# Optimization experiments

Hardware: AMD Instinct MI355X
Metric: run time of the kernel (lower is better)

Reference implementation:

```python
import jax, jax.numpy as jnp
import numpy as np

EOS_ID = 2
PAD_ID = 0


def setup_inputs() -> dict:
    key = jax.random.key(0)
    ks = jax.random.split(key, 10)
    B, E, H, V, T = 64, 512, 512, 32000, 20
    features = jax.random.normal(ks[0], (B, E), dtype=jnp.float32)
    captions = jax.random.randint(ks[1], (B, T), 0, V)            # unused in policy branch
    lengths = jax.random.randint(ks[2], (B,), 1, T + 1)
    lengths = lengths.at[0].set(T)                                 # make max(lengths) == 20 deterministic
    # parameters (match torch init scales roughly)
    embed_W = jax.random.uniform(ks[3], (V, E), jnp.float32, -0.1, 0.1)
    s = 1.0 / np.sqrt(H)
    W_ih = jax.random.uniform(ks[4], (4 * H, E), jnp.float32, -s, s)
    W_hh = jax.random.uniform(ks[5], (4 * H, H), jnp.float32, -s, s)
    b_ih = jax.random.uniform(ks[6], (4 * H,), jnp.float32, -s, s)
    b_hh = jax.random.uniform(ks[7], (4 * H,), jnp.float32, -s, s)
    linear_W = jax.random.uniform(ks[8], (V, H), jnp.float32, -0.1, 0.1)
    linear_b = jnp.zeros((V,), jnp.float32)
    return {"features": features, "captions": captions, "lengths": lengths,
            "use_policy": 1, "embed_W": embed_W, "W_ih": W_ih, "W_hh": W_hh,
            "b_ih": b_ih, "b_hh": b_hh, "linear_W": linear_W, "linear_b": linear_b}


def _lstm_cell(x, h, c, W_ih, W_hh, b_ih, b_hh):
    # PyTorch gate order: i, f, g, o
    gates = x @ W_ih.T + b_ih + h @ W_hh.T + b_hh        # [B, 4H]
    i, f, g, o = jnp.split(gates, 4, axis=-1)
    i, f, o = jax.nn.sigmoid(i), jax.nn.sigmoid(f), jax.nn.sigmoid(o)
    g = jnp.tanh(g)
    c = f * c + i * g
    h = o * jnp.tanh(c)
    return h, c


def reference(features, captions, lengths, use_policy, embed_W, W_ih, W_hh,
              b_ih, b_hh, linear_W, linear_b):
    # LSTM decode with categorical sampling, stopping per-example at EOS (id 2)
    # and padding remaining steps with id 0 / log_prob 0. The original loops
    # over batch and time with batch-size-1 kernels; here we batch + lax.scan.
    B, H = features.shape[0], W_hh.shape[1]
    T = int(jnp.max(lengths))                            # concrete at trace setup
    step_keys = jax.random.split(jax.random.key(42), T)

    def step(carry, key_t):
        h, c, x, done = carry
        h, c = _lstm_cell(x, h, c, W_ih, W_hh, b_ih, b_hh)
        logits = h @ linear_W.T + linear_b               # [B, V]
        logp = jax.nn.log_softmax(logits, axis=-1)
        tok = jax.random.categorical(key_t, logits)      # [B] int32
        lp = jnp.take_along_axis(logp, tok[:, None], axis=1)[:, 0]
        ids_rec = jnp.where(done, PAD_ID, tok)
        lp_rec = jnp.where(done, 0.0, lp)
        done = done | ((tok == EOS_ID) & ~done)          # EOS token itself is recorded
        x = embed_W[tok]                                 # next-step input embedding
        return (h, c, x, done), (ids_rec, lp_rec)

    init = (jnp.zeros((B, H), features.dtype), jnp.zeros((B, H), features.dtype),
            features, jnp.zeros((B,), bool))
    _, (ids, logps) = jax.lax.scan(step, init, step_keys)
    sampled_ids = jnp.transpose(ids)                     # [B, T]
    saved_log_probs = jnp.transpose(logps)               # [B, T]
    return sampled_ids, saved_log_probs
```

## Files before the change

### kernel.cpp

```cpp
#include <hip/hip_runtime.h>
#include <hip/hip_bf16.h>
#include <stdint.h>
#include <float.h>

#define BB 64
#define EE 512
#define HH 512
#define VV 32000
#define TT 20
#define INV2048 0.00048828125f

typedef _Float16 f16x8 __attribute__((ext_vector_type(8)));
typedef float f32x4 __attribute__((ext_vector_type(4)));

__device__ __host__ __forceinline__ void tf2x32(uint32_t k0, uint32_t k1, uint32_t x0, uint32_t x1,
                                                uint32_t& o0, uint32_t& o1) {
  const uint32_t k2 = k0 ^ k1 ^ 0x1BD11BDAu;
  x0 += k0; x1 += k1;
#define RND(R) { x0 += x1; x1 = (x1 << R) | (x1 >> (32 - R)); x1 ^= x0; }
  RND(13) RND(15) RND(26) RND(6)
  x0 += k1; x1 += k2 + 1u;
  RND(17) RND(29) RND(16) RND(24)
  x0 += k2; x1 += k0 + 2u;
  RND(13) RND(15) RND(26) RND(6)
  x0 += k0; x1 += k1 + 3u;
  RND(17) RND(29) RND(16) RND(24)
  x0 += k1; x1 += k2 + 4u;
  RND(13) RND(15) RND(26) RND(6)
  x0 += k2; x1 += k0 + 5u;
#undef RND
  o0 = x0; o1 = x1;
}

__device__ __forceinline__ float gumbel_for(uint32_t k1t, uint32_t k2t, uint32_t idx) {
  uint32_t o0, o1; tf2x32(k1t, k2t, 0u, idx, o0, o1);
  uint32_t bits = o0 ^ o1;
  uint32_t mant = bits >> 9;
  float f = __uint_as_float(0x3f800000u | mant) - 1.0f;
  float u = mant ? f : 1.1754943508222875e-38f;
  return -logf(-logf(u));
}

struct Part { float bv; int bix; float blog; float m; float s; };

__device__ __forceinline__ void part_combine(Part& P, const Part& Q) {
  if (Q.bv > P.bv || (Q.bv == P.bv && Q.bix < P.bix)) { P.bv = Q.bv; P.bix = Q.bix; P.blog = Q.blog; }
  if (Q.m > P.m) { P.s = P.s * expf(P.m - Q.m) + Q.s; P.m = Q.m; }
  else           { P.s += Q.s * expf(Q.m - P.m); }
}

__global__ __launch_bounds__(256) void k_init(float* __restrict__ hA, float* __restrict__ cT,
                                              int* __restrict__ done) {
  int i = blockIdx.x * 256 + threadIdx.x;
  if (i < HH * BB) { hA[i] = 0.f; cT[i] = 0.f; }
  if (i < BB) done[i] = 0;
}

__global__ __launch_bounds__(256) void k_gates(const float* __restrict__ xin,
                                               const float* __restrict__ hT,
                                               const float* __restrict__ Wih,
                                               const float* __restrict__ Whh,
                                               float* __restrict__ gatesP) {
  const int jt = blockIdx.x;
  const int kc = blockIdx.y;
  const int tx = threadIdx.x;
  __shared__ float a[64][64];
  __shared__ float wj[64][68];
  const int bi = (tx & 15) * 4;
  const int ji = (tx >> 4) * 4;
  float acc[4][4] = {};
  const float* Wsrc = (kc < 4) ? Wih : Whh;
  for (int s = 0; s < 2; ++s) {
    const int kg = kc * 128 + s * 64;
    if (kc < 4) {
      #pragma unroll
      for (int r = 0; r < 4; ++r) {
        int fi = r * 256 + tx;
        int b = fi >> 4, k4 = (fi & 15) * 4;
        const float4 v = *(const float4*)(xin + b * EE + kg + k4);
        a[k4 + 0][b] = v.x; a[k4 + 1][b] = v.y; a[k4 + 2][b] = v.z; a[k4 + 3][b] = v.w;
      }
    } else {
      #pragma unroll
      for (int r = 0; r < 4; ++r) {
        int fi = r * 256 + tx;
        int row = fi >> 4, c4 = (fi & 15) * 4;
        *(float4*)(&a[row][c4]) = *(const float4*)(hT + (kg - 512 + row) * BB + c4);
      }
    }
    const int kcol = kg & 511;
    #pragma unroll
    for (int r = 0; r < 4; ++r) {
      int fi = r * 256 + tx;
      int j = fi >> 4, k4 = (fi & 15) * 4;
      const float4 v = *(const float4*)(Wsrc + (size_t)(jt * 64 + j) * EE + kcol + k4);
      wj[k4 + 0][j] = v.x; wj[k4 + 1][j] = v.y; wj[k4 + 2][j] = v.z; wj[k4 + 3][j] = v.w;
    }
    __syncthreads();
    #pragma unroll 8
    for (int kk = 0; kk < 64; ++kk) {
      const float4 av = *(const float4*)(&a[kk][bi]);
      const float4 wv = *(const float4*)(&wj[kk][ji]);
      const float avx[4] = {av.x, av.y, av.z, av.w};
      const float wvx[4] = {wv.x, wv.y, wv.z, wv.w};
      #pragma unroll
      for (int jj = 0; jj < 4; ++jj)
        #pragma unroll
        for (int bb = 0; bb < 4; ++bb)
          acc[jj][bb] = fmaf(wvx[jj], avx[bb], acc[jj][bb]);
    }
    __syncthreads();
  }
  #pragma unroll
  for (int jj = 0; jj < 4; ++jj) {
    float4 o = make_float4(acc[jj][0], acc[jj][1], acc[jj][2], acc[jj][3]);
    *(float4*)(gatesP + ((size_t)kc * 2048 + jt * 64 + ji + jj) * BB + bi) = o;
  }
}

__global__ __launch_bounds__(256) void k_lstm_update(const float* __restrict__ gatesP,
                                                     const float* __restrict__ b_ih,
                                                     const float* __restrict__ b_hh,
                                                     float* __restrict__ cT,
                                                     float* __restrict__ hT) {
  const int blk = blockIdx.x;
  const int tx = threadIdx.x;
  const int b = tx & 63;
  const int dk = tx >> 6;
  #pragma unroll
  for (int r = 0; r < 2; ++r) {
    const int k = blk * 8 + dk + r * 4;
    float g[4];
    #pragma unroll
    for (int gi = 0; gi < 4; ++gi) {
      const int j = gi * 512 + k;
      float s = 0.f;
      #pragma unroll
      for (int kc = 0; kc < 8; ++kc) s += gatesP[((size_t)kc * 2048 + j) * BB + b];
      g[gi] = s + b_ih[j] + b_hh[j];
    }
    const float ig = 1.f / (1.f + expf(-g[0]));
    const float fg = 1.f / (1.f + expf(-g[1]));
    const float gg = tanhf(g[2]);
    const float og = 1.f / (1.f + expf(-g[3]));
    const float c = fg * cT[k * BB + b] + ig * gg;
    cT[k * BB + b] = c;
    hT[k * BB + b] = og * tanhf(c);
  }
}

__global__ __launch_bounds__(256) void k_lstm_update_frag(const float* __restrict__ gatesP,
                                                          const float* __restrict__ b_ih,
                                                          const float* __restrict__ b_hh,
                                                          float* __restrict__ cT,
                                                          float* __restrict__ hT,
                                                          _Float16* __restrict__ hfh,
                                                          _Float16* __restrict__ hfl) {
  const int blk = blockIdx.x;
  const int tx = threadIdx.x;
  const int b = tx & 63;
  const int dk = tx >> 6;
  #pragma unroll
  for (int r = 0; r < 2; ++r) {
    const int k = blk * 8 + dk + r * 4;
    float g[4];
    #pragma unroll
    for (int gi = 0; gi < 4; ++gi) {
      const int j = gi * 512 + k;
      float s = 0.f;
      #pragma unroll
      for (int kc = 0; kc < 8; ++kc) s += gatesP[((size_t)kc * 2048 + j) * BB + b];
      g[gi] = s + b_ih[j] + b_hh[j];
    }
    const float ig = 1.f / (1.f + expf(-g[0]));
    const float fg = 1.f / (1.f + expf(-g[1]));
    const float gg = tanhf(g[2]);
    const float og = 1.f / (1.f + expf(-g[3]));
    const float c = fg * cT[k * BB + b] + ig * gg;
    cT[k * BB + b] = c;
    const float h = og * tanhf(c);
    hT[k * BB + b] = h;
    const _Float16 hh = (_Float16)h;
    const _Float16 hl = (_Float16)((h - (float)hh) * 2048.0f);
    const int cc = k >> 5, kr = k & 31;
    const int lane = (kr >> 3) * 16 + (b & 15), j = kr & 7, nb = b >> 4;
    const int idx = ((cc * 4 + nb) * 64 + lane) * 8 + j;
    hfh[idx] = hh; hfl[idx] = hl;
  }
}

__global__ __launch_bounds__(256) void k_convW(const float* __restrict__ LW,
                                               _Float16* __restrict__ Wh,
                                               _Float16* __restrict__ Wl) {
  const int t = blockIdx.x * 256 + threadIdx.x;
  const int v = t >> 6, kq = t & 63;
  const float4 f0 = *(const float4*)(LW + (size_t)v * HH + kq * 8);
  const float4 f1 = *(const float4*)(LW + (size_t)v * HH + kq * 8 + 4);
  const int vb = v >> 4, m = v & 15;
  const int c = kq >> 2, lh = kq & 3;
  const size_t o = (((size_t)vb * 16 + c) * 64 + lh * 16 + m) * 8;
  const float f[8] = {f0.x, f0.y, f0.z, f0.w, f1.x, f1.y, f1.z, f1.w};
  f16x8 hi, lo;
  #pragma unroll
  for (int j = 0; j < 8; ++j) {
    const _Float16 h = (_Float16)f[j];
    hi[j] = h;
    lo[j] = (_Float16)((f[j] - (float)h) * 2048.0f);
  }
  *(f16x8*)(Wh + o) = hi;
  *(f16x8*)(Wl + o) = lo;
}

__global__ __launch_bounds__(64) void k_logits3(const f16x8* __restrict__ Wh,
                                                const f16x8* __restrict__ Wl,
                                                const f16x8* __restrict__ hfh,
                                                const f16x8* __restrict__ hfl,
                                                const float* __restrict__ lb,
                                                uint32_t k1t, uint32_t k2t,
                                                float4* __restrict__ pf4,
                                                int* __restrict__ pidx) {
  const int vt = blockIdx.x;
  const int lane = threadIdx.x;
  const f32x4 zero = {0.f, 0.f, 0.f, 0.f};
  f32x4 aH[4] = {zero, zero, zero, zero};
  f32x4 aM[4] = {zero, zero, zero, zero};
  #pragma unroll 4
  for (int c = 0; c < 16; ++c) {
    const f16x8 wh = Wh[((size_t)vt * 16 + c) * 64 + lane];
    const f16x8 wl = Wl[((size_t)vt * 16 + c) * 64 + lane];
    #pragma unroll
    for (int nb = 0; nb < 4; ++nb) {
      const f16x8 bh = hfh[(c * 4 + nb) * 64 + lane];
      const f16x8 bl = hfl[(c * 4 + nb) * 64 + lane];
      aH[nb] = __builtin_amdgcn_mfma_f32_16x16x32_f16(wh, bh, aH[nb], 0, 0, 0);
      aM[nb] = __builtin_amdgcn_mfma_f32_16x16x32_f16(wh, bl, aM[nb], 0, 0, 0);
      aM[nb] = __builtin_amdgcn_mfma_f32_16x16x32_f16(wl, bh, aM[nb], 0, 0, 0);
    }
  }
  const int v0 = vt * 16 + ((lane >> 4) << 2);
  const float4 bias = *(const float4*)(lb + v0);
  const float bb4[4] = {bias.x, bias.y, bias.z, bias.w};
  Part P[4];
  #pragma unroll
  for (int nb = 0; nb < 4; ++nb) {
    const int b = nb * 16 + (lane & 15);
    float lg = aH[nb][0] + aM[nb][0] * INV2048 + bb4[0];
    Part p;
    p.bv = lg + gumbel_for(k1t, k2t, (uint32_t)(b * VV + v0));
    p.bix = v0; p.blog = lg; p.m = lg; p.s = 1.0f;
    #pragma unroll
    for (int reg = 1; reg < 4; ++reg) {
      float lg2 = aH[nb][reg] + aM[nb][reg] * INV2048 + bb4[reg];
      float pe = lg2 + gumbel_for(k1t, k2t, (uint32_t)(b * VV + v0 + reg));
      if (pe > p.bv) { p.bv = pe; p.bix = v0 + reg; p.blog = lg2; }
      if (lg2 > p.m) { p.s = p.s * expf(p.m - lg2) + 1.f; p.m = lg2; }
      else           { p.s += expf(lg2 - p.m); }
    }
    P[nb] = p;
  }
  #pragma unroll
  for (int msk = 16; msk <= 32; msk <<= 1) {
    #pragma unroll
    for (int nb = 0; nb < 4; ++nb) {
      Part Q;
      Q.bv   = __shfl_xor(P[nb].bv, msk, 64);
      Q.bix  = __shfl_xor(P[nb].bix, msk, 64);
      Q.blog = __shfl_xor(P[nb].blog, msk, 64);
      Q.m    = __shfl_xor(P[nb].m, msk, 64);
      Q.s    = __shfl_xor(P[nb].s, msk, 64);
      part_combine(P[nb], Q);
    }
  }
  if (lane < 16) {
    #pragma unroll
    for (int nb = 0; nb < 4; ++nb) {
      const int b = nb * 16 + lane;
      pf4[(size_t)vt * BB + b] = make_float4(P[nb].bv, P[nb].blog, P[nb].m, P[nb].s);
      pidx[vt * BB + b] = P[nb].bix;
    }
  }
}

__global__ __launch_bounds__(128) void k_logits2(const float* __restrict__ hT,
                                                 const float* __restrict__ LW,
                                                 const float* __restrict__ lb,
                                                 uint32_t k1t, uint32_t k2t,
                                                 float4* __restrict__ pf4,
                                                 int* __restrict__ pidx) {
  const int vt = blockIdx.x;
  const int tx = threadIdx.x;
  __shared__ float lds[5120];
  float* wTs = lds;
  const int vthr = tx & 15;
  const int bthr = tx >> 4;
  const int vi = vthr * 2;
  const int bi = bthr * 8;
  const int vq = tx >> 4;
  const int ks = tx & 15;
  float acc[2][8] = {};
  for (int kt = 0; kt < 8; ++kt) {
    const int kg = kt * 64;
    #pragma unroll
    for (int s = 0; s < 4; ++s) {
      const int kk = ks + 16 * s;
      const size_t rb = (size_t)(vt * 32 + 4 * vq) * HH + kg + kk;
      float w0 = LW[rb];
      float w1 = LW[rb + HH];
      float w2 = LW[rb + 2 * HH];
      float w3 = LW[rb + 3 * HH];
      const int ph = (4 * vq) ^ (4 * (kk & 7));
      *(float4*)&wTs[kk * 32 + ph] = make_float4(w0, w1, w2, w3);
    }
    __syncthreads();
    #pragma unroll 4
    for (int kk = 0; kk < 64; ++kk) {
      const float* hrow = hT + (size_t)(kg + kk) * BB;
      const float4 h0 = *(const float4*)(hrow + bi);
      const float4 h1 = *(const float4*)(hrow + bi + 4);
      const float2 wv = *(const float2*)&wTs[kk * 32 + (vi ^ (4 * (kk & 7)))];
      acc[0][0] = fmaf(wv.x, h0.x, acc[0][0]); acc[0][1] = fmaf(wv.x, h0.y, acc[0][1]);
      acc[0][2] = fmaf(wv.x, h0.z, acc[0][2]); acc[0][3] = fmaf(wv.x, h0.w, acc[0][3]);
      acc[0][4] = fmaf(wv.x, h1.x, acc[0][4]); acc[0][5] = fmaf(wv.x, h1.y, acc[0][5]);
      acc[0][6] = fmaf(wv.x, h1.z, acc[0][6]); acc[0][7] = fmaf(wv.x, h1.w, acc[0][7]);
      acc[1][0] = fmaf(wv.y, h0.x, acc[1][0]); acc[1][1] = fmaf(wv.y, h0.y, acc[1][1]);
      acc[1][2] = fmaf(wv.y, h0.z, acc[1][2]); acc[1][3] = fmaf(wv.y, h0.w, acc[1][3]);
      acc[1][4] = fmaf(wv.y, h1.x, acc[1][4]); acc[1][5] = fmaf(wv.y, h1.y, acc[1][5]);
      acc[1][6] = fmaf(wv.y, h1.z, acc[1][6]); acc[1][7] = fmaf(wv.y, h1.w, acc[1][7]);
    }
    __syncthreads();
  }
  const int v0g = vt * 32 + vi;
  const float bias0 = lb[v0g];
  const float bias1 = lb[v0g + 1];
  float* red = lds;
  #pragma unroll
  for (int bb = 0; bb < 8; ++bb) {
    const int b = bi + bb;
    const float lg0 = acc[0][bb] + bias0;
    const float lg1 = acc[1][bb] + bias1;
    Part p;
    p.bv = lg0 + gumbel_for(k1t, k2t, (uint32_t)(b * VV + v0g));
    p.bix = v0g; p.blog = lg0;
    const float pe1 = lg1 + gumbel_for(k1t, k2t, (uint32_t)(b * VV + v0g + 1));
    if (pe1 > p.bv) { p.bv = pe1; p.bix = v0g + 1; p.blog = lg1; }
    if (lg0 >= lg1) { p.m = lg0; p.s = 1.f + expf(lg1 - lg0); }
    else            { p.m = lg1; p.s = 1.f + expf(lg0 - lg1); }
    const int slot = (b * 16 + vthr) * 5;
    red[slot + 0] = p.bv; red[slot + 1] = __int_as_float(p.bix); red[slot + 2] = p.blog;
    red[slot + 3] = p.m;  red[slot + 4] = p.s;
  }
  __syncthreads();
  if (tx < 64) {
    const int b = tx;
    Part P;
    { const int s0 = (b * 16) * 5;
      P.bv = red[s0]; P.bix = __float_as_int(red[s0 + 1]); P.blog = red[s0 + 2];
      P.m = red[s0 + 3]; P.s = red[s0 + 4]; }
    #pragma unroll
    for (int c = 1; c < 16; ++c) {
      const int s0 = (b * 16 + c) * 5;
      Part Q; Q.bv = red[s0]; Q.bix = __float_as_int(red[s0 + 1]); Q.blog = red[s0 + 2];
      Q.m = red[s0 + 3]; Q.s = red[s0 + 4];
      part_combine(P, Q);
    }
    pf4[(size_t)vt * BB + b] = make_float4(P.bv, P.blog, P.m, P.s);
    pidx[vt * BB + b] = P.bix;
  }
}

__global__ __launch_bounds__(256) void k_sample2(const float4* __restrict__ pf4,
                                                 const int* __restrict__ pidx,
                                                 const float* __restrict__ embW,
                                                 int* __restrict__ done,
                                                 float* __restrict__ x,
                                                 float* __restrict__ out,
                                                 int step, int nvt) {
  const int b = blockIdx.x;
  const int tx = threadIdx.x;
  __shared__ float red[256 * 5];
  __shared__ int stok;
  Part p; p.bv = -FLT_MAX; p.bix = 0x7fffffff; p.blog = 0.f; p.m = -FLT_MAX; p.s = 0.f;
  for (int vt = tx; vt < nvt; vt += 256) {
    float4 q = pf4[(size_t)vt * BB + b];
    Part Q; Q.bv = q.x; Q.blog = q.y; Q.m = q.z; Q.s = q.w; Q.bix = pidx[vt * BB + b];
    part_combine(p, Q);
  }
  red[tx * 5 + 0] = p.bv; red[tx * 5 + 1] = __int_as_float(p.bix); red[tx * 5 + 2] = p.blog;
  red[tx * 5 + 3] = p.m;  red[tx * 5 + 4] = p.s;
  __syncthreads();
  for (int st = 128; st > 0; st >>= 1) {
    if (tx < st) {
      const int s0 = tx * 5, s1 = (tx + st) * 5;
      Part P, Q;
      P.bv = red[s0]; P.bix = __float_as_int(red[s0 + 1]); P.blog = red[s0 + 2]; P.m = red[s0 + 3]; P.s = red[s0 + 4];
      Q.bv = red[s1]; Q.bix = __float_as_int(red[s1 + 1]); Q.blog = red[s1 + 2]; Q.m = red[s1 + 3]; Q.s = red[s1 + 4];
      part_combine(P, Q);
      red[s0] = P.bv; red[s0 + 1] = __int_as_float(P.bix); red[s0 + 2] = P.blog; red[s0 + 3] = P.m; red[s0 + 4] = P.s;
    }
    __syncthreads();
  }
  if (tx == 0) {
    const int tok = __float_as_int(red[1]);
    const float blog = red[2], M = red[3], S = red[4];
    const float lp = blog - (M + logf(S));
    const int dn = done[b];
    out[b * TT + step] = dn ? 0.0f : (float)tok;
    out[BB * TT + b * TT + step] = dn ? 0.0f : lp;
    done[b] = dn | (tok == 2);
    stok = tok;
  }
  __syncthreads();
  const int tok = stok;
  for (int e = tx; e < EE; e += 256) x[b * EE + e] = embW[(size_t)tok * EE + e];
}

extern "C" void kernel_launch(void* const* d_in, const int* in_sizes, int n_in,
                              void* d_out, int out_size, void* d_ws, size_t ws_size,
                              hipStream_t stream) {
  const float* features = (const float*)d_in[0];
  const float* embW     = (const float*)d_in[4];
  const float* Wih      = (const float*)d_in[5];
  const float* Whh      = (const float*)d_in[6];
  const float* bih      = (const float*)d_in[7];
  const float* bhh      = (const float*)d_in[8];
  const float* LW       = (const float*)d_in[9];
  const float* lb       = (const float*)d_in[10];
  float* out = (float*)d_out;

  uint32_t keys[TT][2];
  for (int t = 0; t < TT; ++t) tf2x32(0u, 42u, 0u, (uint32_t)t, keys[t][0], keys[t][1]);

  float* ws = (float*)d_ws;
  float* hA = ws;
  float* hB = ws + 32768;
  float* cT = ws + 65536;
  float* x  = ws + 98304;

  if (ws_size >= (size_t)73000000) {
    float*  gatesP = ws + 131072;
    float4* pf4    = (float4*)(ws + 1179648);
    int*    pidx   = (int*)(ws + 1691648);
    int*    done   = (int*)(ws + 1819648);
    _Float16* hfh  = (_Float16*)(ws + 1819712);
    _Float16* hfl  = (_Float16*)(ws + 1836096);
    _Float16* Whi  = (_Float16*)(ws + 1852480);
    _Float16* Wlo  = (_Float16*)(ws + 10044480);

    k_convW<<<dim3(8000), dim3(256), 0, stream>>>(LW, Whi, Wlo);
    k_init<<<dim3(128), dim3(256), 0, stream>>>(hA, cT, done);
    const float* hin = hA;
    float* hout = hB;
    for (int t = 0; t < TT; ++t) {
      const float* xin = (t == 0) ? features : x;
      k_gates<<<dim3(32, 8), dim3(256), 0, stream>>>(xin, hin, Wih, Whh, gatesP);
      k_lstm_update_frag<<<dim3(64), dim3(256), 0, stream>>>(gatesP, bih, bhh, cT, hout, hfh, hfl);
      k_logits3<<<dim3(2000), dim3(64), 0, stream>>>((const f16x8*)Whi, (const f16x8*)Wlo,
                                                     (const f16x8*)hfh, (const f16x8*)hfl,
                                                     lb, keys[t][0], keys[t][1], pf4, pidx);
      k_sample2<<<dim3(64), dim3(256), 0, stream>>>(pf4, pidx, embW, done, x, out, t, 2000);
      const float* tmp = hout; hout = (float*)hin; hin = tmp;
    }
  } else {
    float*  gatesP = ws + 131072;
    float4* pf4    = (float4*)(ws + 131072 + 1048576);
    int*    pidx   = (int*)(ws + 131072 + 1048576 + 256000);
    int*    done   = (int*)(ws + 131072 + 1048576 + 256000 + 64000);

    k_init<<<dim3(128), dim3(256), 0, stream>>>(hA, cT, done);
    const float* hin = hA;
    float* hout = hB;
    for (int t = 0; t < TT; ++t) {
      const float* xin = (t == 0) ? features : x;
      k_gates<<<dim3(32, 8), dim3(256), 0, stream>>>(xin, hin, Wih, Whh, gatesP);
      k_lstm_update<<<dim3(64), dim3(256), 0, stream>>>(gatesP, bih, bhh, cT, hout);
      k_logits2<<<dim3(1000), dim3(128), 0, stream>>>(hout, LW, lb, keys[t][0], keys[t][1], pf4, pidx);
      k_sample2<<<dim3(64), dim3(256), 0, stream>>>(pf4, pidx, embW, done, x, out, t, 1000);
      const float* tmp = hout; hout = (float*)hin; hin = tmp;
    }
  }
}
```

Before: 1.112 ms.

## Use 4-wave logits blocks with in-block reduction and LDS-staged weight conversion

The logits kernel now runs four waves per block, each handling one 16-vocab tile. The waves combine their partial softmax/argmax results through LDS, so only 500 partials per batch row go to the sampling kernel instead of 2000. It also prefetches the next weight chunk in registers and splits the middle-term MFMA accumulators into two chains to shorten dependency stalls. The weight conversion kernel stages tiles through LDS so its global reads and writes coalesce. In exchange the logits kernel adds a __syncthreads, LDS use and more registers per block.

```diff
diff --git a/kernel.cpp b/kernel.cpp
--- a/kernel.cpp
+++ b/kernel.cpp
@@ -189,53 +189,72 @@
   }
 }
 
-__global__ __launch_bounds__(256) void k_convW(const float* __restrict__ LW,
-                                               _Float16* __restrict__ Wh,
-                                               _Float16* __restrict__ Wl) {
-  const int t = blockIdx.x * 256 + threadIdx.x;
-  const int v = t >> 6, kq = t & 63;
-  const float4 f0 = *(const float4*)(LW + (size_t)v * HH + kq * 8);
-  const float4 f1 = *(const float4*)(LW + (size_t)v * HH + kq * 8 + 4);
-  const int vb = v >> 4, m = v & 15;
-  const int c = kq >> 2, lh = kq & 3;
-  const size_t o = (((size_t)vb * 16 + c) * 64 + lh * 16 + m) * 8;
-  const float f[8] = {f0.x, f0.y, f0.z, f0.w, f1.x, f1.y, f1.z, f1.w};
-  f16x8 hi, lo;
-  #pragma unroll
-  for (int j = 0; j < 8; ++j) {
-    const _Float16 h = (_Float16)f[j];
-    hi[j] = h;
-    lo[j] = (_Float16)((f[j] - (float)h) * 2048.0f);
-  }
-  *(f16x8*)(Wh + o) = hi;
-  *(f16x8*)(Wl + o) = lo;
-}
-
-__global__ __launch_bounds__(64) void k_logits3(const f16x8* __restrict__ Wh,
-                                                const f16x8* __restrict__ Wl,
-                                                const f16x8* __restrict__ hfh,
-                                                const f16x8* __restrict__ hfl,
-                                                const float* __restrict__ lb,
-                                                uint32_t k1t, uint32_t k2t,
-                                                float4* __restrict__ pf4,
-                                                int* __restrict__ pidx) {
-  const int vt = blockIdx.x;
-  const int lane = threadIdx.x;
+__global__ __launch_bounds__(256) void k_convW2(const float* __restrict__ LW,
+                                                _Float16* __restrict__ Wh,
+                                                _Float16* __restrict__ Wl) {
+  const int bv = blockIdx.x, bk = blockIdx.y;
+  const int tx = threadIdx.x;
+  __shared__ float lds[64][65];
+  #pragma unroll
+  for (int r = 0; r < 4; ++r) {
+    const int fi = r * 256 + tx;
+    const int vl = fi >> 4, k4 = (fi & 15) * 4;
+    const float4 v = *(const float4*)(LW + (size_t)(bv * 64 + vl) * HH + bk * 64 + k4);
+    lds[vl][k4] = v.x; lds[vl][k4 + 1] = v.y; lds[vl][k4 + 2] = v.z; lds[vl][k4 + 3] = v.w;
+  }
+  __syncthreads();
+  #pragma unroll
+  for (int r = 0; r < 2; ++r) {
+    const int u = r * 256 + tx;
+    const int frag = u >> 6;
+    const int vbl = frag >> 1, cl = frag & 1;
+    const int lane = u & 63;
+    const int m = lane & 15, lh = lane >> 4;
+    f16x8 hi, lo;
+    #pragma unroll
+    for (int j = 0; j < 8; ++j) {
+      const float f = lds[vbl * 16 + m][cl * 32 + lh * 8 + j];
+      const _Float16 h = (_Float16)f;
+      hi[j] = h;
+      lo[j] = (_Float16)((f - (float)h) * 2048.0f);
+    }
+    const size_t o = (((size_t)(bv * 4 + vbl) * 16 + (bk * 2 + cl)) * 64 + lane) * 8;
+    *(f16x8*)(Wh + o) = hi;
+    *(f16x8*)(Wl + o) = lo;
+  }
+}
+
+__global__ __launch_bounds__(256) void k_logits4(const f16x8* __restrict__ Wh,
+                                                 const f16x8* __restrict__ Wl,
+                                                 const f16x8* __restrict__ hfh,
+                                                 const f16x8* __restrict__ hfl,
+                                                 const float* __restrict__ lb,
+                                                 uint32_t k1t, uint32_t k2t,
+                                                 float4* __restrict__ pf4,
+                                                 int* __restrict__ pidx) {
+  const int wv = threadIdx.x >> 6;
+  const int vt = blockIdx.x * 4 + wv;
+  const int lane = threadIdx.x & 63;
+  __shared__ float red[4][64][5];
   const f32x4 zero = {0.f, 0.f, 0.f, 0.f};
-  f32x4 aH[4] = {zero, zero, zero, zero};
-  f32x4 aM[4] = {zero, zero, zero, zero};
+  f32x4 aH[4]  = {zero, zero, zero, zero};
+  f32x4 aM1[4] = {zero, zero, zero, zero};
+  f32x4 aM2[4] = {zero, zero, zero, zero};
+  const size_t wbase = (size_t)vt * 16 * 64 + lane;
+  f16x8 whC = Wh[wbase], wlC = Wl[wbase];
   #pragma unroll 4
   for (int c = 0; c < 16; ++c) {
-    const f16x8 wh = Wh[((size_t)vt * 16 + c) * 64 + lane];
-    const f16x8 wl = Wl[((size_t)vt * 16 + c) * 64 + lane];
+    f16x8 whN, wlN;
+    if (c < 15) { whN = Wh[wbase + (c + 1) * 64]; wlN = Wl[wbase + (c + 1) * 64]; }
     #pragma unroll
     for (int nb = 0; nb < 4; ++nb) {
       const f16x8 bh = hfh[(c * 4 + nb) * 64 + lane];
       const f16x8 bl = hfl[(c * 4 + nb) * 64 + lane];
-      aH[nb] = __builtin_amdgcn_mfma_f32_16x16x32_f16(wh, bh, aH[nb], 0, 0, 0);
-      aM[nb] = __builtin_amdgcn_mfma_f32_16x16x32_f16(wh, bl, aM[nb], 0, 0, 0);
-      aM[nb] = __builtin_amdgcn_mfma_f32_16x16x32_f16(wl, bh, aM[nb], 0, 0, 0);
-    }
+      aH[nb]  = __builtin_amdgcn_mfma_f32_16x16x32_f16(whC, bh, aH[nb], 0, 0, 0);
+      aM1[nb] = __builtin_amdgcn_mfma_f32_16x16x32_f16(whC, bl, aM1[nb], 0, 0, 0);
+      aM2[nb] = __builtin_amdgcn_mfma_f32_16x16x32_f16(wlC, bh, aM2[nb], 0, 0, 0);
+    }
+    whC = whN; wlC = wlN;
   }
   const int v0 = vt * 16 + ((lane >> 4) << 2);
   const float4 bias = *(const float4*)(lb + v0);
@@ -244,13 +263,13 @@
   #pragma unroll
   for (int nb = 0; nb < 4; ++nb) {
     const int b = nb * 16 + (lane & 15);
-    float lg = aH[nb][0] + aM[nb][0] * INV2048 + bb4[0];
+    float lg = aH[nb][0] + (aM1[nb][0] + aM2[nb][0]) * INV2048 + bb4[0];
     Part p;
     p.bv = lg + gumbel_for(k1t, k2t, (uint32_t)(b * VV + v0));
     p.bix = v0; p.blog = lg; p.m = lg; p.s = 1.0f;
     #pragma unroll
     for (int reg = 1; reg < 4; ++reg) {
-      float lg2 = aH[nb][reg] + aM[nb][reg] * INV2048 + bb4[reg];
+      float lg2 = aH[nb][reg] + (aM1[nb][reg] + aM2[nb][reg]) * INV2048 + bb4[reg];
       float pe = lg2 + gumbel_for(k1t, k2t, (uint32_t)(b * VV + v0 + reg));
       if (pe > p.bv) { p.bv = pe; p.bix = v0 + reg; p.blog = lg2; }
       if (lg2 > p.m) { p.s = p.s * expf(p.m - lg2) + 1.f; p.m = lg2; }
@@ -275,9 +294,25 @@
     #pragma unroll
     for (int nb = 0; nb < 4; ++nb) {
       const int b = nb * 16 + lane;
-      pf4[(size_t)vt * BB + b] = make_float4(P[nb].bv, P[nb].blog, P[nb].m, P[nb].s);
-      pidx[vt * BB + b] = P[nb].bix;
-    }
+      red[wv][b][0] = P[nb].bv; red[wv][b][1] = __int_as_float(P[nb].bix);
+      red[wv][b][2] = P[nb].blog; red[wv][b][3] = P[nb].m; red[wv][b][4] = P[nb].s;
+    }
+  }
+  __syncthreads();
+  if (threadIdx.x < 64) {
+    const int b = threadIdx.x;
+    Part Pc;
+    Pc.bv = red[0][b][0]; Pc.bix = __float_as_int(red[0][b][1]); Pc.blog = red[0][b][2];
+    Pc.m = red[0][b][3]; Pc.s = red[0][b][4];
+    #pragma unroll
+    for (int w = 1; w < 4; ++w) {
+      Part Q;
+      Q.bv = red[w][b][0]; Q.bix = __float_as_int(red[w][b][1]); Q.blog = red[w][b][2];
+      Q.m = red[w][b][3]; Q.s = red[w][b][4];
+      part_combine(Pc, Q);
+    }
+    pf4[(size_t)blockIdx.x * BB + b] = make_float4(Pc.bv, Pc.blog, Pc.m, Pc.s);
+    pidx[blockIdx.x * BB + b] = Pc.bix;
   }
 }
 
@@ -446,7 +481,7 @@
     _Float16* Whi  = (_Float16*)(ws + 1852480);
     _Float16* Wlo  = (_Float16*)(ws + 10044480);
 
-    k_convW<<<dim3(8000), dim3(256), 0, stream>>>(LW, Whi, Wlo);
+    k_convW2<<<dim3(500, 8), dim3(256), 0, stream>>>(LW, Whi, Wlo);
     k_init<<<dim3(128), dim3(256), 0, stream>>>(hA, cT, done);
     const float* hin = hA;
     float* hout = hB;
@@ -454,10 +489,10 @@
       const float* xin = (t == 0) ? features : x;
       k_gates<<<dim3(32, 8), dim3(256), 0, stream>>>(xin, hin, Wih, Whh, gatesP);
       k_lstm_update_frag<<<dim3(64), dim3(256), 0, stream>>>(gatesP, bih, bhh, cT, hout, hfh, hfl);
-      k_logits3<<<dim3(2000), dim3(64), 0, stream>>>((const f16x8*)Whi, (const f16x8*)Wlo,
+      k_logits4<<<dim3(500), dim3(256), 0, stream>>>((const f16x8*)Whi, (const f16x8*)Wlo,
                                                      (const f16x8*)hfh, (const f16x8*)hfl,
                                                      lb, keys[t][0], keys[t][1], pf4, pidx);
-      k_sample2<<<dim3(64), dim3(256), 0, stream>>>(pf4, pidx, embW, done, x, out, t, 2000);
+      k_sample2<<<dim3(64), dim3(256), 0, stream>>>(pf4, pidx, embW, done, x, out, t, 500);
       const float* tmp = hout; hout = (float*)hin; hin = tmp;
     }
   } else {
```

Result: faster. 935.3 us (median of 2 runs) (-15.9%).
